# Kernel optimization log

Measured on AMD Instinct MI355X. Metric: run time of the kernel, lower is better.

The kernel has to match this reference:

```python
import jax, jax.numpy as jnp
import numpy as np

N_NODES = 100000
N_EDGES = 3200000
N_FEAT = 128
EMBED = 20
N_CLASSES = 10
N_GRAPHS = 64


def setup_inputs() -> dict:
    key = jax.random.key(0)
    ks = jax.random.split(key, 8)
    x = jax.random.normal(ks[0], (N_NODES, N_FEAT), dtype=jnp.float32)
    edge_index = jax.random.randint(ks[1], (2, N_EDGES), 0, N_NODES, dtype=jnp.int64)
    edge_weights = jax.random.uniform(ks[2], (N_EDGES,), dtype=jnp.float32)
    batch = jnp.sort(jax.random.randint(ks[3], (N_NODES,), 0, N_GRAPHS, dtype=jnp.int64))
    # GCNConv parameters (glorot-ish scale) and final linear layer
    W = jax.random.normal(ks[4], (N_FEAT, EMBED), dtype=jnp.float32) * (1.0 / np.sqrt(N_FEAT))
    b = jnp.zeros((EMBED,), dtype=jnp.float32)
    lin_W = jax.random.normal(ks[5], (2 * EMBED, N_CLASSES), dtype=jnp.float32) * (1.0 / np.sqrt(2 * EMBED))
    lin_b = jnp.zeros((N_CLASSES,), dtype=jnp.float32)
    return {"x": x, "edge_index": edge_index, "edge_weights": edge_weights,
            "batch": batch, "W": W, "b": b, "lin_W": lin_W, "lin_b": lin_b}


def reference(x, edge_index, edge_weights, batch, W, b, lin_W, lin_b):
    N = x.shape[0]
    # --- GCNConv with self-loops and symmetric normalization (PyG semantics) ---
    loops = jnp.arange(N, dtype=edge_index.dtype)
    src = jnp.concatenate([edge_index[0], loops])
    dst = jnp.concatenate([edge_index[1], loops])
    w = jnp.concatenate([edge_weights, jnp.ones((N,), dtype=edge_weights.dtype)])
    deg = jax.ops.segment_sum(w, dst, num_segments=N)  # degree at targets
    dinv = jnp.where(deg > 0, jax.lax.rsqrt(deg), 0.0)
    norm = dinv[src] * w * dinv[dst]  # [E+N]
    xw = x @ W  # [N, EMBED]
    msg = xw[src] * norm[:, None]  # gather + scale
    out1 = jax.ops.segment_sum(msg, dst, num_segments=N) + b  # scatter-add
    # --- L2 normalize per node (F.normalize p=2 dim=1, eps=1e-12), then ReLU ---
    nrm = jnp.sqrt(jnp.sum(out1 * out1, axis=1, keepdims=True))
    embed = jax.nn.relu(out1 / jnp.maximum(nrm, 1e-12))
    # --- global max / mean pool per graph ---
    mx = jax.ops.segment_max(embed, batch, num_segments=N_GRAPHS)
    mx = jnp.where(jnp.isfinite(mx), mx, 0.0)  # empty graphs -> 0
    cnt = jax.ops.segment_sum(jnp.ones((N,), dtype=embed.dtype), batch, num_segments=N_GRAPHS)
    mean = jax.ops.segment_sum(embed, batch, num_segments=N_GRAPHS) / jnp.maximum(cnt, 1.0)[:, None]
    pooled = jnp.concatenate([mx, mean], axis=-1)  # [G, 2*EMBED]
    return pooled @ lin_W + lin_b
```

## Files before the change

kernel.cpp:

```cpp
#include <hip/hip_runtime.h>
#include <hip/hip_fp16.h>

#define NN 100000
#define NE 3200000
#define NF 128
#define EM 20
#define NC 10
#define NG 64

#define NB 782
#define CAPB 4608
#define T 4096
#define SBLK 1024

__global__ __launch_bounds__(SBLK) void k_scatter(
        const int* __restrict__ src, const int* __restrict__ dst,
        const float* __restrict__ w, int* __restrict__ gcursor,
        uint2* __restrict__ barr) {
    __shared__ unsigned int cnt[1024];
    __shared__ unsigned int off[1024];
    __shared__ unsigned int gbase[NB];
    __shared__ unsigned int wsum[16];
    __shared__ uint2 staged[T];
    __shared__ unsigned short bkt[T];
    int tid = threadIdx.x;
    long E0 = (long)blockIdx.x * T;
    int tot = (int)min((long)T, (long)NE - E0);
    cnt[tid] = 0;
    __syncthreads();
    unsigned int dreg[T / SBLK];
#pragma unroll
    for (int k = 0; k < T / SBLK; ++k) {
        int e = k * SBLK + tid;
        dreg[k] = 0;
        if (e < tot) {
            dreg[k] = (unsigned)dst[E0 + e];
            atomicAdd(&cnt[dreg[k] >> 7], 1u);
        }
    }
    __syncthreads();
    {
        int lane = tid & 63, wv = tid >> 6;
        unsigned int v = cnt[tid];
        unsigned int s = v;
#pragma unroll
        for (int o = 1; o < 64; o <<= 1) {
            unsigned int t = __shfl_up(s, o);
            if (lane >= o) s += t;
        }
        if (lane == 63) wsum[wv] = s;
        __syncthreads();
        if (tid == 0) {
            unsigned int a = 0;
#pragma unroll
            for (int i = 0; i < 16; ++i) { unsigned int t = wsum[i]; wsum[i] = a; a += t; }
        }
        __syncthreads();
        off[tid] = wsum[wv] + s - v;
    }
    __syncthreads();
    if (tid < NB) {
        unsigned int c = cnt[tid];
        gbase[tid] = c ? (unsigned int)atomicAdd(&gcursor[tid], (int)c) : 0u;
        cnt[tid] = 0;
    }
    __syncthreads();
#pragma unroll
    for (int k = 0; k < T / SBLK; ++k) {
        int e = k * SBLK + tid;
        if (e < tot) {
            long ge = E0 + e;
            unsigned int d = dreg[k];
            unsigned int b = d >> 7;
            unsigned int slot = atomicAdd(&cnt[b], 1u);
            unsigned int pos = off[b] + slot;
            staged[pos] = make_uint2((((unsigned)src[ge]) << 7) | (d & 127u),
                                     __float_as_uint(w[ge]));
            bkt[pos] = (unsigned short)b;
        }
    }
    __syncthreads();
    for (int i = tid; i < tot; i += SBLK) {
        unsigned int b = bkt[i];
        unsigned int gpos = gbase[b] + ((unsigned)i - off[b]);
        if (gpos < CAPB) barr[(size_t)b * CAPB + gpos] = staged[i];
    }
}

__global__ __launch_bounds__(512, 8) void k_degxw(
        const int* __restrict__ gcursor, const uint2* __restrict__ barr,
        const float* __restrict__ x, const float* __restrict__ W,
        float* __restrict__ dinv,
        __half* __restrict__ xwhA, __half* __restrict__ xwhB) {
    __shared__ float Ws[NF * EM];
    __shared__ float dacc[128];
    __shared__ float dvs[128];
    int bk = blockIdx.x, tid = threadIdx.x;
    if (tid < 128) dacc[tid] = 0.f;
    for (int i = tid; i < NF * EM; i += 512) Ws[i] = W[i];
    __syncthreads();
    int base = bk * 128;
    int cntb = min(gcursor[bk], CAPB);
    const uint2* row = barr + (size_t)bk * CAPB;
    for (int i = tid; i < cntb; i += 512) {
        uint2 r = row[i];
        atomicAdd(&dacc[r.x & 127u], __uint_as_float(r.y));
    }
    int n = tid & 127;
    int jg = tid >> 7;
    int j0 = jg * 5;
    int node = base + n;
    float acc[5] = {0.f, 0.f, 0.f, 0.f, 0.f};
    if (node < NN) {
        const float4* xr = (const float4*)(x + (size_t)node * NF);
        for (int k4 = 0; k4 < NF / 4; ++k4) {
            float4 xc = xr[k4];
            const float* wr = Ws + (k4 * 4) * EM + j0;
#pragma unroll
            for (int jj = 0; jj < 5; ++jj) acc[jj] = fmaf(xc.x, wr[jj], acc[jj]);
            wr += EM;
#pragma unroll
            for (int jj = 0; jj < 5; ++jj) acc[jj] = fmaf(xc.y, wr[jj], acc[jj]);
            wr += EM;
#pragma unroll
            for (int jj = 0; jj < 5; ++jj) acc[jj] = fmaf(xc.z, wr[jj], acc[jj]);
            wr += EM;
#pragma unroll
            for (int jj = 0; jj < 5; ++jj) acc[jj] = fmaf(xc.w, wr[jj], acc[jj]);
        }
    }
    __syncthreads();
    if (tid < 128) {
        float dv = rsqrtf(1.0f + dacc[tid]);
        dvs[tid] = dv;
        int gd = base + tid;
        if (gd < NN) dinv[gd] = dv;
    }
    __syncthreads();
    if (node < NN) {
        float dv = dvs[n];
#pragma unroll
        for (int jj = 0; jj < 5; ++jj) {
            int j = j0 + jj;
            __half hv = __float2half(acc[jj] * dv);
            if (j < 16) xwhA[(size_t)node * 16 + j] = hv;
            else        xwhB[(size_t)node * 4 + (j - 16)] = hv;
        }
    }
}

__device__ inline void unpack16(uint4 a0, uint4 a1, float* f) {
    const __half2* h = (const __half2*)&a0;
#pragma unroll
    for (int c = 0; c < 4; ++c) { float2 t = __half22float2(h[c]); f[2*c] = t.x; f[2*c+1] = t.y; }
    h = (const __half2*)&a1;
#pragma unroll
    for (int c = 0; c < 4; ++c) { float2 t = __half22float2(h[c]); f[8+2*c] = t.x; f[9+2*c] = t.y; }
}
__device__ inline void unpack4(uint2 b0, float* f) {
    const __half2* h = (const __half2*)&b0;
#pragma unroll
    for (int c = 0; c < 2; ++c) { float2 t = __half22float2(h[c]); f[2*c] = t.x; f[2*c+1] = t.y; }
}

__global__ void k_sortaggr(const int* __restrict__ gcursor,
                           const unsigned long long* __restrict__ barr64,
                           const __half* __restrict__ xwhA, const __half* __restrict__ xwhB,
                           const float* __restrict__ dinv, const float* __restrict__ b,
                           float* __restrict__ embed) {
    __shared__ unsigned long long srt[CAPB];
    __shared__ unsigned int cnt[128];
    __shared__ unsigned int off[128];
    __shared__ unsigned int wtot;
    int bk = blockIdx.x, tid = threadIdx.x;
    if (tid < 128) cnt[tid] = 0;
    __syncthreads();
    int cntb = min(gcursor[bk], CAPB);
    const unsigned long long* row = barr64 + (size_t)bk * CAPB;
    unsigned long long rec[9];
    unsigned int pos[9];
    int K = 0;
    for (int e = tid; e < cntb; e += 512) {
        rec[K] = row[e];
        pos[K] = atomicAdd(&cnt[(unsigned)rec[K] & 127u], 1u);
        ++K;
    }
    __syncthreads();
    unsigned int v = 0, s = 0;
    if (tid < 128) {
        v = cnt[tid]; s = v;
#pragma unroll
        for (int o = 1; o < 64; o <<= 1) {
            unsigned int t = __shfl_up(s, o);
            if ((tid & 63) >= o) s += t;
        }
        if (tid == 63) wtot = s;
    }
    __syncthreads();
    if (tid < 128) {
        if (tid >= 64) s += wtot;
        off[tid] = s;
    }
    __syncthreads();
    for (int k = 0; k < K; ++k) {
        unsigned int dl = (unsigned)rec[k] & 127u;
        srt[off[dl] - cnt[dl] + pos[k]] = rec[k];
    }
    __syncthreads();
    int d = tid >> 2, sub = tid & 3;
    int s0 = (int)(off[d] - cnt[d]), s1 = (int)off[d];
    const uint4* pA = (const uint4*)xwhA;
    const uint2* pB = (const uint2*)xwhB;
    float acc[20];
#pragma unroll
    for (int j = 0; j < 20; ++j) acc[j] = 0.f;
    for (int e = s0 + sub; e < s1; e += 4) {
        unsigned long long r = srt[e];
        unsigned int sN = ((unsigned int)r) >> 7;
        float nw = __uint_as_float((unsigned int)(r >> 32));
        uint4 a0 = pA[(size_t)sN * 2];
        uint4 a1 = pA[(size_t)sN * 2 + 1];
        uint2 b0 = pB[sN];
        float f[20];
        unpack16(a0, a1, f);
        unpack4(b0, f + 16);
#pragma unroll
        for (int j = 0; j < 20; ++j) acc[j] = fmaf(f[j], nw, acc[j]);
    }
#pragma unroll
    for (int j = 0; j < 20; ++j) {
        acc[j] += __shfl_xor(acc[j], 1);
        acc[j] += __shfl_xor(acc[j], 2);
    }
    if (sub == 0) {
        int gd = bk * 128 + d;
        if (gd < NN) {
            float dv = dinv[gd];
            uint4 a0 = pA[(size_t)gd * 2];
            uint4 a1 = pA[(size_t)gd * 2 + 1];
            uint2 b0 = pB[gd];
            float xdh[20];
            unpack16(a0, a1, xdh);
            unpack4(b0, xdh + 16);
            float r[20];
            float ss = 0.f;
#pragma unroll
            for (int j = 0; j < 20; ++j) {
                r[j] = dv * (acc[j] + xdh[j]) + b[j];
                ss = fmaf(r[j], r[j], ss);
            }
            float inv = 1.0f / fmaxf(sqrtf(ss), 1e-12f);
            float4 o4[5];
            float* o = (float*)o4;
#pragma unroll
            for (int j = 0; j < 20; ++j) {
                float e2 = r[j] * inv;
                o[j] = e2 > 0.f ? e2 : 0.f;
            }
            float4* eo = (float4*)(embed + (size_t)gd * EM);
#pragma unroll
            for (int c = 0; c < 5; ++c) eo[c] = o4[c];
        }
    }
}

__device__ inline int lbound(const int* __restrict__ batch, int key) {
    int lo = 0, hi = NN;
    while (lo < hi) {
        int mid = (lo + hi) >> 1;
        if (batch[mid] < key) lo = mid + 1; else hi = mid;
    }
    return lo;
}

__global__ void k_poolfinal(const float* __restrict__ embed, const int* __restrict__ batch,
                            const float* __restrict__ lw, const float* __restrict__ lb,
                            float* __restrict__ out) {
    __shared__ float cross[4][40];
    __shared__ float pooled[40];
    int g = blockIdx.x;
    int s0 = lbound(batch, g), s1 = lbound(batch, g + 1);
    int cnt = s1 - s0;
    float mx[EM], sm[EM];
#pragma unroll
    for (int j = 0; j < EM; ++j) { mx[j] = 0.f; sm[j] = 0.f; }
    for (int n = s0 + threadIdx.x; n < s1; n += 256) {
        const float4* e = (const float4*)(embed + (size_t)n * EM);
#pragma unroll
        for (int c = 0; c < 5; ++c) {
            float4 v = e[c];
            int j = c * 4;
            mx[j+0] = fmaxf(mx[j+0], v.x); sm[j+0] += v.x;
            mx[j+1] = fmaxf(mx[j+1], v.y); sm[j+1] += v.y;
            mx[j+2] = fmaxf(mx[j+2], v.z); sm[j+2] += v.z;
            mx[j+3] = fmaxf(mx[j+3], v.w); sm[j+3] += v.w;
        }
    }
#pragma unroll
    for (int o = 32; o > 0; o >>= 1) {
#pragma unroll
        for (int j = 0; j < EM; ++j) {
            mx[j] = fmaxf(mx[j], __shfl_xor(mx[j], o));
            sm[j] += __shfl_xor(sm[j], o);
        }
    }
    int wave = threadIdx.x >> 6, lane = threadIdx.x & 63;
    if (lane == 0) {
#pragma unroll
        for (int j = 0; j < EM; ++j) { cross[wave][j] = mx[j]; cross[wave][EM + j] = sm[j]; }
    }
    __syncthreads();
    if (threadIdx.x < 40) {
        int j = threadIdx.x;
        float v = cross[0][j];
        if (j < EM) v = fmaxf(fmaxf(v, cross[1][j]), fmaxf(cross[2][j], cross[3][j]));
        else        v = v + cross[1][j] + cross[2][j] + cross[3][j];
        if (j >= EM) v *= 1.0f / fmaxf((float)cnt, 1.0f);
        pooled[j] = v;
    }
    __syncthreads();
    if (threadIdx.x < NC) {
        int c = threadIdx.x;
        float acc = lb[c];
#pragma unroll
        for (int j = 0; j < 2 * EM; ++j) acc = fmaf(pooled[j], lw[j * NC + c], acc);
        out[g * NC + c] = acc;
    }
}

static inline size_t align_up(size_t v) { return (v + 1023) & ~(size_t)1023; }

extern "C" void kernel_launch(void* const* d_in, const int* in_sizes, int n_in,
                              void* d_out, int out_size, void* d_ws, size_t ws_size,
                              hipStream_t stream) {
    const float* x     = (const float*)d_in[0];
    const int*   ei    = (const int*)d_in[1];
    const float* ew    = (const float*)d_in[2];
    const int*   batch = (const int*)d_in[3];
    const float* W     = (const float*)d_in[4];
    const float* b     = (const float*)d_in[5];
    const float* lw    = (const float*)d_in[6];
    const float* lb    = (const float*)d_in[7];
    float* out = (float*)d_out;

    char* ws = (char*)d_ws;
    int*    gcursor = (int*)ws;    ws += align_up(4096);
    float*  dinv    = (float*)ws;  ws += align_up((size_t)NN * 4);
    __half* xwhA    = (__half*)ws; ws += align_up((size_t)NN * 16 * 2);
    __half* xwhB    = (__half*)ws; ws += align_up((size_t)NN * 4 * 2);
    float*  embed   = (float*)ws;  ws += align_up((size_t)NN * EM * 4);
    uint2*  barr    = (uint2*)ws;
    unsigned long long* barr64 = (unsigned long long*)barr;

    const int* srcp = ei;
    const int* dstp = ei + NE;

    (void)hipMemsetAsync(gcursor, 0, 4096, stream);
    k_scatter<<<(NE + T - 1) / T, SBLK, 0, stream>>>(srcp, dstp, ew, gcursor, barr);
    k_degxw<<<NB, 512, 0, stream>>>(gcursor, barr, x, W, dinv, xwhA, xwhB);
    k_sortaggr<<<NB, 512, 0, stream>>>(gcursor, barr64, xwhA, xwhB, dinv, b, embed);
    k_poolfinal<<<NG, 256, 0, stream>>>(embed, batch, lw, lb, out);
}
```

Before: 262.8 us.

## Fuse x@W GEMV into scatter kernel as extra blocks, slim degree kernel

Moves the dense x@W projection out of the degree kernel and into extra blocks of the edge-scatter launch, so the compute-bound matvec can overlap with the memory-bound bucketing pass. The projection result goes to an fp32 scratch buffer, which is reused for embed. The degree kernel now only accumulates degrees and rescales and converts the projected features to half. The cost is an extra fp32 write and read of the projection, plus shared-memory aliasing in the fused kernel.

```diff
diff --git a/kernel.cpp b/kernel.cpp
--- a/kernel.cpp
+++ b/kernel.cpp
@@ -12,19 +12,55 @@
 #define CAPB 4608
 #define T 4096
 #define SBLK 1024
-
-__global__ __launch_bounds__(SBLK) void k_scatter(
+#define NXW 391
+
+__global__ __launch_bounds__(SBLK) void k_scatfat(
         const int* __restrict__ src, const int* __restrict__ dst,
         const float* __restrict__ w, int* __restrict__ gcursor,
-        uint2* __restrict__ barr) {
-    __shared__ unsigned int cnt[1024];
-    __shared__ unsigned int off[1024];
-    __shared__ unsigned int gbase[NB];
-    __shared__ unsigned int wsum[16];
-    __shared__ uint2 staged[T];
-    __shared__ unsigned short bkt[T];
+        uint2* __restrict__ barr,
+        const float* __restrict__ x, const float* __restrict__ W,
+        float* __restrict__ xwf) {
+    __shared__ __align__(16) char smem[52352];
     int tid = threadIdx.x;
-    long E0 = (long)blockIdx.x * T;
+
+    if (blockIdx.x < NXW) {
+        float* Ws = (float*)smem;
+        for (int i = tid; i < NF * EM; i += SBLK) Ws[i] = W[i];
+        __syncthreads();
+        int node = blockIdx.x * 256 + (tid >> 2);
+        int j0 = (tid & 3) * 5;
+        if (node >= NN) return;
+        float acc[5] = {0.f, 0.f, 0.f, 0.f, 0.f};
+        const float4* xr = (const float4*)(x + (size_t)node * NF);
+        for (int k4 = 0; k4 < NF / 4; ++k4) {
+            float4 xc = xr[k4];
+            const float* wr = Ws + (k4 * 4) * EM + j0;
+#pragma unroll
+            for (int jj = 0; jj < 5; ++jj) acc[jj] = fmaf(xc.x, wr[jj], acc[jj]);
+            wr += EM;
+#pragma unroll
+            for (int jj = 0; jj < 5; ++jj) acc[jj] = fmaf(xc.y, wr[jj], acc[jj]);
+            wr += EM;
+#pragma unroll
+            for (int jj = 0; jj < 5; ++jj) acc[jj] = fmaf(xc.z, wr[jj], acc[jj]);
+            wr += EM;
+#pragma unroll
+            for (int jj = 0; jj < 5; ++jj) acc[jj] = fmaf(xc.w, wr[jj], acc[jj]);
+        }
+        float* o = xwf + (size_t)node * EM + j0;
+#pragma unroll
+        for (int jj = 0; jj < 5; ++jj) o[jj] = acc[jj];
+        return;
+    }
+
+    unsigned int* cnt   = (unsigned int*)smem;
+    unsigned int* off   = (unsigned int*)(smem + 4096);
+    unsigned int* gbase = (unsigned int*)(smem + 8192);
+    unsigned int* wsum  = (unsigned int*)(smem + 11320);
+    uint2*        staged= (uint2*)(smem + 11384);
+    unsigned short* bkt = (unsigned short*)(smem + 44152);
+
+    long E0 = (long)(blockIdx.x - NXW) * T;
     int tot = (int)min((long)T, (long)NE - E0);
     cnt[tid] = 0;
     __syncthreads();
@@ -87,64 +123,36 @@
     }
 }
 
-__global__ __launch_bounds__(512, 8) void k_degxw(
+__global__ __launch_bounds__(1024) void k_degps(
         const int* __restrict__ gcursor, const uint2* __restrict__ barr,
-        const float* __restrict__ x, const float* __restrict__ W,
-        float* __restrict__ dinv,
+        const float* xwf, float* __restrict__ dinv,
         __half* __restrict__ xwhA, __half* __restrict__ xwhB) {
-    __shared__ float Ws[NF * EM];
     __shared__ float dacc[128];
     __shared__ float dvs[128];
     int bk = blockIdx.x, tid = threadIdx.x;
     if (tid < 128) dacc[tid] = 0.f;
-    for (int i = tid; i < NF * EM; i += 512) Ws[i] = W[i];
-    __syncthreads();
-    int base = bk * 128;
+    __syncthreads();
     int cntb = min(gcursor[bk], CAPB);
     const uint2* row = barr + (size_t)bk * CAPB;
-    for (int i = tid; i < cntb; i += 512) {
+    for (int i = tid; i < cntb; i += 1024) {
         uint2 r = row[i];
         atomicAdd(&dacc[r.x & 127u], __uint_as_float(r.y));
-    }
-    int n = tid & 127;
-    int jg = tid >> 7;
-    int j0 = jg * 5;
-    int node = base + n;
-    float acc[5] = {0.f, 0.f, 0.f, 0.f, 0.f};
-    if (node < NN) {
-        const float4* xr = (const float4*)(x + (size_t)node * NF);
-        for (int k4 = 0; k4 < NF / 4; ++k4) {
-            float4 xc = xr[k4];
-            const float* wr = Ws + (k4 * 4) * EM + j0;
-#pragma unroll
-            for (int jj = 0; jj < 5; ++jj) acc[jj] = fmaf(xc.x, wr[jj], acc[jj]);
-            wr += EM;
-#pragma unroll
-            for (int jj = 0; jj < 5; ++jj) acc[jj] = fmaf(xc.y, wr[jj], acc[jj]);
-            wr += EM;
-#pragma unroll
-            for (int jj = 0; jj < 5; ++jj) acc[jj] = fmaf(xc.z, wr[jj], acc[jj]);
-            wr += EM;
-#pragma unroll
-            for (int jj = 0; jj < 5; ++jj) acc[jj] = fmaf(xc.w, wr[jj], acc[jj]);
-        }
     }
     __syncthreads();
     if (tid < 128) {
         float dv = rsqrtf(1.0f + dacc[tid]);
         dvs[tid] = dv;
-        int gd = base + tid;
+        int gd = bk * 128 + tid;
         if (gd < NN) dinv[gd] = dv;
     }
     __syncthreads();
-    if (node < NN) {
-        float dv = dvs[n];
-#pragma unroll
-        for (int jj = 0; jj < 5; ++jj) {
-            int j = j0 + jj;
-            __half hv = __float2half(acc[jj] * dv);
-            if (j < 16) xwhA[(size_t)node * 16 + j] = hv;
-            else        xwhB[(size_t)node * 4 + (j - 16)] = hv;
+    for (int i = tid; i < 128 * EM; i += 1024) {
+        int n = i / EM, dim = i - n * EM;
+        int gd = bk * 128 + n;
+        if (gd < NN) {
+            __half hv = __float2half(xwf[(size_t)gd * EM + dim] * dvs[n]);
+            if (dim < 16) xwhA[(size_t)gd * 16 + dim] = hv;
+            else          xwhB[(size_t)gd * 4 + (dim - 16)] = hv;
         }
     }
 }
@@ -167,7 +175,7 @@
                            const unsigned long long* __restrict__ barr64,
                            const __half* __restrict__ xwhA, const __half* __restrict__ xwhB,
                            const float* __restrict__ dinv, const float* __restrict__ b,
-                           float* __restrict__ embed) {
+                           float* embed) {
     __shared__ unsigned long long srt[CAPB];
     __shared__ unsigned int cnt[128];
     __shared__ unsigned int off[128];
@@ -348,16 +356,18 @@
     float*  dinv    = (float*)ws;  ws += align_up((size_t)NN * 4);
     __half* xwhA    = (__half*)ws; ws += align_up((size_t)NN * 16 * 2);
     __half* xwhB    = (__half*)ws; ws += align_up((size_t)NN * 4 * 2);
-    float*  embed   = (float*)ws;  ws += align_up((size_t)NN * EM * 4);
+    float*  xwf     = (float*)ws;  ws += align_up((size_t)NN * EM * 4);
     uint2*  barr    = (uint2*)ws;
     unsigned long long* barr64 = (unsigned long long*)barr;
+    float*  embed   = xwf;
 
     const int* srcp = ei;
     const int* dstp = ei + NE;
 
     (void)hipMemsetAsync(gcursor, 0, 4096, stream);
-    k_scatter<<<(NE + T - 1) / T, SBLK, 0, stream>>>(srcp, dstp, ew, gcursor, barr);
-    k_degxw<<<NB, 512, 0, stream>>>(gcursor, barr, x, W, dinv, xwhA, xwhB);
+    k_scatfat<<<NXW + (NE + T - 1) / T, SBLK, 0, stream>>>(srcp, dstp, ew, gcursor, barr,
+                                                           x, W, xwf);
+    k_degps<<<NB, 1024, 0, stream>>>(gcursor, barr, xwf, dinv, xwhA, xwhB);
     k_sortaggr<<<NB, 512, 0, stream>>>(gcursor, barr64, xwhA, xwhB, dinv, b, embed);
     k_poolfinal<<<NG, 256, 0, stream>>>(embed, batch, lw, lb, out);
 }
```

Result: faster. 238.4 us (-9.3%).
